# Performance work log

Hardware: AMD Instinct MI355X
Metric: run time of the kernel (lower is better)

Reference implementation:

```python
import jax, jax.numpy as jnp
import numpy as np

EMB = 256
T = 32          # block_size (hardcoded causal mask length)
HEAD = 128      # total head_size
NH = 8          # n_heads
DH = HEAD // NH # 16 per-head size
B = 4096
EPS = 1e-5


def _ln(x, g, b):
    mu = jnp.mean(x, -1, keepdims=True)
    var = jnp.var(x, -1, keepdims=True)
    return (x - mu) * jax.lax.rsqrt(var + EPS) * g + b


def setup_inputs() -> dict:
    key = jax.random.key(0)
    ks = jax.random.split(key, 12)
    s_in = 1.0 / np.sqrt(EMB)
    s_h = 1.0 / np.sqrt(HEAD)
    s_ff = 1.0 / np.sqrt(4 * EMB)
    return {
        "X": jax.random.normal(ks[0], (B, T, EMB), jnp.float32),
        "ln_g": jnp.ones((EMB,), jnp.float32),
        "ln_b": jnp.zeros((EMB,), jnp.float32),
        # per-head Q/K/V projections packed: [EMB, HEAD] == concat of NH [EMB, DH] heads
        "Wq": jax.random.uniform(ks[1], (EMB, HEAD), jnp.float32, -s_in, s_in),
        "bq": jax.random.uniform(ks[2], (HEAD,), jnp.float32, -s_in, s_in),
        "Wk": jax.random.uniform(ks[3], (EMB, HEAD), jnp.float32, -s_in, s_in),
        "bk": jax.random.uniform(ks[4], (HEAD,), jnp.float32, -s_in, s_in),
        "Wv": jax.random.uniform(ks[5], (EMB, HEAD), jnp.float32, -s_in, s_in),
        "bv": jax.random.uniform(ks[6], (HEAD,), jnp.float32, -s_in, s_in),
        "Wo": jax.random.uniform(ks[7], (HEAD, EMB), jnp.float32, -s_h, s_h),
        "bo": jax.random.uniform(ks[8], (EMB,), jnp.float32, -s_h, s_h),
        "W1": jax.random.uniform(ks[9], (EMB, 4 * EMB), jnp.float32, -s_in, s_in),
        "b1": jax.random.uniform(ks[10], (4 * EMB,), jnp.float32, -s_in, s_in),
        "W2": jax.random.uniform(ks[11], (4 * EMB, EMB), jnp.float32, -s_ff, s_ff),
        "b2": jax.random.uniform(jax.random.fold_in(key, 99), (EMB,), jnp.float32, -s_ff, s_ff),
    }


def reference(X, ln_g, ln_b, Wq, bq, Wk, bk, Wv, bv, Wo, bo, W1, b1, W2, b2):
    h = _ln(X, ln_g, ln_b)                              # [B,T,E]
    # packed QKV, split into heads: [B,T,NH,DH]
    Q = (h @ Wq + bq).reshape(B, T, NH, DH)
    K = (h @ Wk + bk).reshape(B, T, NH, DH)
    V = (h @ Wv + bv).reshape(B, T, NH, DH)
    scores = jnp.einsum("bqhd,bkhd->bhqk", Q, K)        # [B,NH,T,T]
    mask = jnp.tril(jnp.ones((T, T), bool))
    # original: masked_fill(-inf) then divide by sqrt(dh); -inf unchanged
    scores = jnp.where(mask, scores / np.sqrt(DH), -jnp.inf)
    attn = jax.nn.softmax(scores, -1)
    ctx = jnp.einsum("bhqk,bkhd->bqhd", attn, V).reshape(B, T, HEAD)
    X = ctx @ Wo + bo + X                               # residual 1
    h2 = _ln(X, ln_g, ln_b)                             # shared LN params
    out = jax.nn.relu(h2 @ W1 + b1) @ W2 + b2 + X       # residual 2
    return out
```

## Files before the change

kernel.cpp:

```cpp
#include <hip/hip_runtime.h>
#include <math.h>

typedef __attribute__((ext_vector_type(8))) __bf16 bf16x8;
typedef __attribute__((ext_vector_type(8))) unsigned short u16x8;
typedef __attribute__((ext_vector_type(4))) unsigned short u16x4;
typedef __attribute__((ext_vector_type(4))) float f32x4;

namespace {
constexpr int EMB = 256;
constexpr int HD  = 128;
constexpr int FF  = 1024;
constexpr float EPSV = 1e-5f;
constexpr int M   = 64;

constexpr int WS_QKV = 0;
constexpr int WS_O   = 98304;
constexpr int WS_1   = 131072;
constexpr int WS_2   = 393216;

__device__ __forceinline__ unsigned short f32_to_bf16(float f) {
    unsigned int u = __builtin_bit_cast(unsigned int, f);
    u += 0x7FFFu + ((u >> 16) & 1u);
    return (unsigned short)(u >> 16);
}
__device__ __forceinline__ float bf16_to_f32(unsigned short h) {
    return __builtin_bit_cast(float, ((unsigned int)h) << 16);
}
__device__ __forceinline__ f32x4 mfma16(u16x8 a, u16x8 b, f32x4 c) {
    return __builtin_amdgcn_mfma_f32_16x16x32_bf16(
        __builtin_bit_cast(bf16x8, a), __builtin_bit_cast(bf16x8, b), c, 0, 0, 0);
}
__device__ __forceinline__ int swzB(int row) { return (row & 7) << 4; }

__device__ __forceinline__ u16x8 ldsA256(const unsigned short* base, int row, int k0) {
    int byte = (row * 256 + k0 * 2) ^ swzB(row);
    return *(const u16x8*)((const char*)base + byte);
}
__device__ __forceinline__ u16x8 ldsA512(const unsigned short* base, int row, int k0) {
    int byte = (row * 512 + k0 * 2) ^ swzB(row);
    return *(const u16x8*)((const char*)base + byte);
}
__device__ __forceinline__ u16x8 ldgF(const unsigned short* base, int frag, int lane) {
    return *(const u16x8*)(base + ((size_t)frag * 64 + lane) * 8);
}
}

__global__ __launch_bounds__(256) void wconv(
    const float* __restrict__ Wq, const float* __restrict__ Wk, const float* __restrict__ Wv,
    const float* __restrict__ Wo, const float* __restrict__ W1, const float* __restrict__ W2,
    unsigned short* __restrict__ ws) {
    int e = blockIdx.x * 256 + threadIdx.x;
    int j, lane, kk, nt, n, k;
    float v;
    if (e < WS_O) {
        int t = e; j = t & 7; lane = (t >> 3) & 63; int r2 = t >> 9;
        kk = r2 & 7; nt = r2 >> 3;
        n = nt * 16 + (lane & 15); k = kk * 32 + (lane >> 4) * 8 + j;
        const float* W = (n < 128) ? Wq : ((n < 256) ? Wk : Wv);
        v = W[k * HD + (n & 127)];
    } else if (e < WS_1) {
        int t = e - WS_O; j = t & 7; lane = (t >> 3) & 63; int r2 = t >> 9;
        kk = r2 & 3; nt = r2 >> 2;
        n = nt * 16 + (lane & 15); k = kk * 32 + (lane >> 4) * 8 + j;
        v = Wo[k * EMB + n];
    } else if (e < WS_2) {
        int t = e - WS_1; j = t & 7; lane = (t >> 3) & 63; int r2 = t >> 9;
        kk = r2 & 7; nt = r2 >> 3;
        n = nt * 16 + (lane & 15); k = kk * 32 + (lane >> 4) * 8 + j;
        v = W1[k * FF + n];
    } else {
        int t = e - WS_2; j = t & 7; lane = (t >> 3) & 63; int r2 = t >> 9;
        kk = r2 & 31; nt = r2 >> 5;
        n = nt * 16 + (lane & 15); k = kk * 32 + (lane >> 4) * 8 + j;
        v = W2[k * EMB + n];
    }
    ws[e] = f32_to_bf16(v);
}

__global__ __launch_bounds__(256, 1) void attn_block_mfma(
    const float* __restrict__ X, const float* __restrict__ ln_g, const float* __restrict__ ln_b,
    const float* __restrict__ bq, const float* __restrict__ bk, const float* __restrict__ bv,
    const float* __restrict__ bo, const float* __restrict__ b1, const float* __restrict__ b2,
    const unsigned short* __restrict__ ws, float* __restrict__ out) {
    __shared__ __attribute__((aligned(16))) char smem[81920];
    unsigned short* hbuf = (unsigned short*)smem;
    unsigned short* Qb   = (unsigned short*)(smem + 32768);
    char* Kc             = smem + 49152;
    char* Vc             = smem + 65536;
    unsigned short* X1b  = (unsigned short*)(smem + 49152);
    unsigned short* fch  = Qb;

    const unsigned short* WTqkv = ws + WS_QKV;
    const unsigned short* WTo   = ws + WS_O;
    const unsigned short* WT1   = ws + WS_1;
    const unsigned short* WT2   = ws + WS_2;

    const int tid  = threadIdx.x;
    const int wv   = tid >> 6;
    const int lane = tid & 63;
    const int lr   = lane & 15;
    const int lh   = lane >> 4;
    const int row0 = blockIdx.x * M;
    const f32x4 Z  = {0.f, 0.f, 0.f, 0.f};

    {
        const int r = tid >> 3, sub = tid & 7;
        #pragma unroll 1
        for (int pass = 0; pass < 2; ++pass) {
            int rr = pass * 32 + r;
            const float* xr = X + (size_t)(row0 + rr) * EMB;
            float4 vv[8];
            float s = 0.f, ss = 0.f;
            #pragma unroll
            for (int j = 0; j < 8; ++j) {
                float4 v = *(const float4*)&xr[sub * 4 + j * 32];
                vv[j] = v;
                s  += (v.x + v.y) + (v.z + v.w);
                ss += (v.x * v.x + v.y * v.y) + (v.z * v.z + v.w * v.w);
            }
            #pragma unroll
            for (int w = 1; w < 8; w <<= 1) { s += __shfl_xor(s, w, 64); ss += __shfl_xor(ss, w, 64); }
            float mu  = s * (1.f / EMB);
            float inv = rsqrtf(fmaxf(ss * (1.f / EMB) - mu * mu, 0.f) + EPSV);
            #pragma unroll
            for (int j = 0; j < 8; ++j) {
                int c = sub * 4 + j * 32;
                float4 v = vv[j];
                float4 g4 = *(const float4*)&ln_g[c];
                float4 b4 = *(const float4*)&ln_b[c];
                u16x4 pk;
                pk[0] = f32_to_bf16((v.x - mu) * inv * g4.x + b4.x);
                pk[1] = f32_to_bf16((v.y - mu) * inv * g4.y + b4.y);
                pk[2] = f32_to_bf16((v.z - mu) * inv * g4.z + b4.z);
                pk[3] = f32_to_bf16((v.w - mu) * inv * g4.w + b4.w);
                *(u16x4*)((char*)hbuf + ((rr * 512 + c * 2) ^ swzB(rr))) = pk;
            }
        }
    }
    __syncthreads();

    {
        #pragma unroll 1
        for (int mtp = 0; mtp < 4; mtp += 2) {
            u16x8 afr[2][8];
            #pragma unroll
            for (int m = 0; m < 2; ++m)
                #pragma unroll
                for (int kk = 0; kk < 8; ++kk)
                    afr[m][kk] = ldsA512(hbuf, (mtp + m) * 16 + lr, kk * 32 + lh * 8);
            #pragma unroll 1
            for (int i = 0; i < 6; ++i) {
                int nt = wv * 6 + i;
                u16x8 bfr[8];
                #pragma unroll
                for (int kk = 0; kk < 8; ++kk) bfr[kk] = ldgF(WTqkv, nt * 8 + kk, lane);
                int gcol = nt * 16 + lr;
                int mat = gcol >> 7, c = gcol & 127;
                const float* bias = (mat == 0) ? bq : ((mat == 1) ? bk : bv);
                float bc = bias[c];
                char* regbase = smem + 32768 + mat * 16384;
                #pragma unroll
                for (int m = 0; m < 2; ++m) {
                    f32x4 e = Z, o = Z;
                    #pragma unroll
                    for (int kk = 0; kk < 8; kk += 2) {
                        e = mfma16(afr[m][kk], bfr[kk], e);
                        o = mfma16(afr[m][kk + 1], bfr[kk + 1], o);
                    }
                    f32x4 a = e + o;
                    #pragma unroll
                    for (int reg = 0; reg < 4; ++reg) {
                        int r0 = (mtp + m) * 16 + lh * 4 + reg;
                        *(unsigned short*)(regbase + ((r0 * 256 + c * 2) ^ swzB(r0))) =
                            f32_to_bf16(a[reg] + bc);
                    }
                }
            }
        }
    }
    __syncthreads();

    {
        const int hd = (tid >> 5) & 7, q = tid & 31;
        #pragma unroll 1
        for (int s = 0; s < 2; ++s) {
            int row = s * 32 + q;
            int by0 = (row * 256 + hd * 32) ^ swzB(row);
            int by1 = (row * 256 + hd * 32 + 16) ^ swzB(row);
            float qreg[16];
            {
                u16x8 a = *(const u16x8*)((const char*)Qb + by0);
                u16x8 b_ = *(const u16x8*)((const char*)Qb + by1);
                #pragma unroll
                for (int j = 0; j < 8; ++j) { qreg[j] = bf16_to_f32(a[j]); qreg[8 + j] = bf16_to_f32(b_[j]); }
            }
            float p[32]; float mmax = -1e30f;
            #pragma unroll
            for (int k = 0; k < 32; ++k) {
                int rk = s * 32 + k;
                int kb0 = (rk * 256 + hd * 32) ^ swzB(rk);
                int kb1 = (rk * 256 + hd * 32 + 16) ^ swzB(rk);
                u16x8 a = *(const u16x8*)(Kc + kb0);
                u16x8 b_ = *(const u16x8*)(Kc + kb1);
                float s_ = 0.f;
                #pragma unroll
                for (int j = 0; j < 8; ++j)
                    s_ += qreg[j] * bf16_to_f32(a[j]) + qreg[8 + j] * bf16_to_f32(b_[j]);
                s_ *= 0.25f;
                p[k] = s_;
                if (k <= q) mmax = fmaxf(mmax, s_);
            }
            float den = 0.f;
            #pragma unroll
            for (int k = 0; k < 32; ++k) {
                float e = (k <= q) ? __expf(p[k] - mmax) : 0.f;
                p[k] = e; den += e;
            }
            float rd = 1.f / den;
            float ctx[16];
            #pragma unroll
            for (int j = 0; j < 16; ++j) ctx[j] = 0.f;
            #pragma unroll
            for (int k = 0; k < 32; ++k) {
                int rk = s * 32 + k;
                int vb0 = (rk * 256 + hd * 32) ^ swzB(rk);
                int vb1 = (rk * 256 + hd * 32 + 16) ^ swzB(rk);
                u16x8 a = *(const u16x8*)(Vc + vb0);
                u16x8 b_ = *(const u16x8*)(Vc + vb1);
                float pk_ = p[k];
                #pragma unroll
                for (int j = 0; j < 8; ++j) { ctx[j] += pk_ * bf16_to_f32(a[j]); ctx[8 + j] += pk_ * bf16_to_f32(b_[j]); }
            }
            u16x8 o0, o1;
            #pragma unroll
            for (int j = 0; j < 8; ++j) { o0[j] = f32_to_bf16(ctx[j] * rd); o1[j] = f32_to_bf16(ctx[8 + j] * rd); }
            *(u16x8*)((char*)Qb + by0) = o0;
            *(u16x8*)((char*)Qb + by1) = o1;
        }
    }
    __syncthreads();

    {
        u16x8 afr[4][4];
        #pragma unroll
        for (int mt = 0; mt < 4; ++mt)
            #pragma unroll
            for (int kk = 0; kk < 4; ++kk)
                afr[mt][kk] = ldsA256(Qb, mt * 16 + lr, kk * 32 + lh * 8);
        #pragma unroll 1
        for (int i = 0; i < 4; ++i) {
            int nt = wv * 4 + i;
            u16x8 bfr[4];
            #pragma unroll
            for (int kk = 0; kk < 4; ++kk) bfr[kk] = ldgF(WTo, nt * 4 + kk, lane);
            int col = nt * 16 + lr;
            float bc = bo[col];
            #pragma unroll
            for (int mt = 0; mt < 4; ++mt) {
                f32x4 e = Z, o = Z;
                e = mfma16(afr[mt][0], bfr[0], e);
                o = mfma16(afr[mt][1], bfr[1], o);
                e = mfma16(afr[mt][2], bfr[2], e);
                o = mfma16(afr[mt][3], bfr[3], o);
                f32x4 a = e + o;
                #pragma unroll
                for (int reg = 0; reg < 4; ++reg) {
                    int r0 = mt * 16 + lh * 4 + reg;
                    float xv = X[(size_t)(row0 + r0) * EMB + col];
                    *(unsigned short*)((char*)X1b + ((r0 * 512 + col * 2) ^ swzB(r0))) =
                        f32_to_bf16(a[reg] + bc + xv);
                }
            }
        }
    }
    __syncthreads();

    {
        const int r = tid >> 3, sub = tid & 7;
        #pragma unroll 1
        for (int pass = 0; pass < 2; ++pass) {
            int rr = pass * 32 + r;
            float vals[32];
            float s = 0.f, ss = 0.f;
            #pragma unroll
            for (int j = 0; j < 8; ++j) {
                int c = sub * 4 + j * 32;
                u16x4 hv = *(const u16x4*)((const char*)X1b + ((rr * 512 + c * 2) ^ swzB(rr)));
                #pragma unroll
                for (int t = 0; t < 4; ++t) {
                    float f = bf16_to_f32(hv[t]);
                    vals[j * 4 + t] = f;
                    s += f; ss += f * f;
                }
            }
            #pragma unroll
            for (int w = 1; w < 8; w <<= 1) { s += __shfl_xor(s, w, 64); ss += __shfl_xor(ss, w, 64); }
            float mu  = s * (1.f / EMB);
            float inv = rsqrtf(fmaxf(ss * (1.f / EMB) - mu * mu, 0.f) + EPSV);
            #pragma unroll
            for (int j = 0; j < 8; ++j) {
                int c = sub * 4 + j * 32;
                float4 g4 = *(const float4*)&ln_g[c];
                float4 b4 = *(const float4*)&ln_b[c];
                u16x4 pk;
                pk[0] = f32_to_bf16((vals[j * 4 + 0] - mu) * inv * g4.x + b4.x);
                pk[1] = f32_to_bf16((vals[j * 4 + 1] - mu) * inv * g4.y + b4.y);
                pk[2] = f32_to_bf16((vals[j * 4 + 2] - mu) * inv * g4.z + b4.z);
                pk[3] = f32_to_bf16((vals[j * 4 + 3] - mu) * inv * g4.w + b4.w);
                *(u16x4*)((char*)hbuf + ((rr * 512 + c * 2) ^ swzB(rr))) = pk;
            }
        }
    }
    __syncthreads();

    {
        f32x4 acc2[4][4];
        #pragma unroll
        for (int mt = 0; mt < 4; ++mt)
            #pragma unroll
            for (int i = 0; i < 4; ++i) acc2[mt][i] = Z;

        #pragma unroll 1
        for (int ch = 0; ch < 8; ++ch) {
            #pragma unroll 1
            for (int mtp = 0; mtp < 4; mtp += 2) {
                u16x8 afr[2][8];
                #pragma unroll
                for (int m = 0; m < 2; ++m)
                    #pragma unroll
                    for (int kk = 0; kk < 8; ++kk)
                        afr[m][kk] = ldsA512(hbuf, (mtp + m) * 16 + lr, kk * 32 + lh * 8);
                #pragma unroll
                for (int f = 0; f < 2; ++f) {
                    int fn = ch * 8 + wv * 2 + f;
                    u16x8 bAll[8];
                    #pragma unroll
                    for (int kk = 0; kk < 8; ++kk) bAll[kk] = ldgF(WT1, fn * 8 + kk, lane);
                    float bc = b1[fn * 16 + lr];
                    int cc = (wv * 2 + f) * 16 + lr;
                    #pragma unroll
                    for (int m = 0; m < 2; ++m) {
                        f32x4 e = Z, o = Z;
                        #pragma unroll
                        for (int kk = 0; kk < 8; kk += 2) {
                            e = mfma16(afr[m][kk], bAll[kk], e);
                            o = mfma16(afr[m][kk + 1], bAll[kk + 1], o);
                        }
                        f32x4 a = e + o;
                        #pragma unroll
                        for (int reg = 0; reg < 4; ++reg) {
                            int r0 = (mtp + m) * 16 + lh * 4 + reg;
                            *(unsigned short*)((char*)fch + ((r0 * 256 + cc * 2) ^ swzB(r0))) =
                                f32_to_bf16(fmaxf(a[reg] + bc, 0.f));
                        }
                    }
                }
            }
            __syncthreads();
            u16x8 b2f[4][4];
            #pragma unroll
            for (int i = 0; i < 4; ++i)
                #pragma unroll
                for (int kk = 0; kk < 4; ++kk)
                    b2f[i][kk] = ldgF(WT2, (wv * 4 + i) * 32 + ch * 4 + kk, lane);
            #pragma unroll
            for (int mt = 0; mt < 4; ++mt) {
                u16x8 afr[4];
                #pragma unroll
                for (int kk = 0; kk < 4; ++kk)
                    afr[kk] = ldsA256(fch, mt * 16 + lr, kk * 32 + lh * 8);
                #pragma unroll
                for (int i = 0; i < 4; ++i) {
                    f32x4 t = acc2[mt][i];
                    t = mfma16(afr[0], b2f[i][0], t);
                    t = mfma16(afr[1], b2f[i][1], t);
                    t = mfma16(afr[2], b2f[i][2], t);
                    t = mfma16(afr[3], b2f[i][3], t);
                    acc2[mt][i] = t;
                }
            }
            __syncthreads();
        }
        float* outp = out + (size_t)row0 * EMB;
        #pragma unroll
        for (int i = 0; i < 4; ++i) {
            int col = (wv * 4 + i) * 16 + lr;
            float bc = b2[col];
            #pragma unroll
            for (int mt = 0; mt < 4; ++mt) {
                #pragma unroll
                for (int reg = 0; reg < 4; ++reg) {
                    int r0 = mt * 16 + lh * 4 + reg;
                    float x1 = bf16_to_f32(*(const unsigned short*)((const char*)X1b +
                                          ((r0 * 512 + col * 2) ^ swzB(r0))));
                    outp[(size_t)r0 * EMB + col] = acc2[mt][i][reg] + bc + x1;
                }
            }
        }
    }
}

extern "C" void kernel_launch(void* const* d_in, const int* in_sizes, int n_in,
                              void* d_out, int out_size, void* d_ws, size_t ws_size,
                              hipStream_t stream) {
    const float* X    = (const float*)d_in[0];
    const float* ln_g = (const float*)d_in[1];
    const float* ln_b = (const float*)d_in[2];
    const float* Wq   = (const float*)d_in[3];
    const float* bq   = (const float*)d_in[4];
    const float* Wk   = (const float*)d_in[5];
    const float* bk   = (const float*)d_in[6];
    const float* Wv   = (const float*)d_in[7];
    const float* bv   = (const float*)d_in[8];
    const float* Wo   = (const float*)d_in[9];
    const float* bo   = (const float*)d_in[10];
    const float* W1   = (const float*)d_in[11];
    const float* b1   = (const float*)d_in[12];
    const float* W2   = (const float*)d_in[13];
    const float* b2   = (const float*)d_in[14];
    unsigned short* ws = (unsigned short*)d_ws;
    float* O = (float*)d_out;

    wconv<<<2560, 256, 0, stream>>>(Wq, Wk, Wv, Wo, W1, W2, ws);
    attn_block_mfma<<<2048, 256, 0, stream>>>(X, ln_g, ln_b, bq, bk, bv, bo, b1, b2, ws, O);
}
```

Before: 431.6 us.

## Split fused block into attention and FFN kernels with smaller per-kernel LDS

Splits the single fused kernel into two: an attention kernel that handles one 32-row sequence per block and writes the fp32 residual X1 to the output buffer, and an FFN kernel that reads X1 back from global memory, applies LayerNorm and the MLP, and adds the residual in place. Each kernel uses much less LDS (40KB and 48KB instead of 80KB), so more workgroups can be resident per CU. This costs an extra global round-trip of the B*T*EMB fp32 intermediate and one more launch. It also replaces the manual bf16 rounding with a native __bf16 conversion and keeps X1 in fp32 rather than bf16, which slightly changes numerics.

Measured after the change: 500.2 us. +15.9%, slower.

```diff
diff --git a/kernel.cpp b/kernel.cpp
--- a/kernel.cpp
+++ b/kernel.cpp
@@ -11,7 +11,6 @@
 constexpr int HD  = 128;
 constexpr int FF  = 1024;
 constexpr float EPSV = 1e-5f;
-constexpr int M   = 64;
 
 constexpr int WS_QKV = 0;
 constexpr int WS_O   = 98304;
@@ -19,9 +18,7 @@
 constexpr int WS_2   = 393216;
 
 __device__ __forceinline__ unsigned short f32_to_bf16(float f) {
-    unsigned int u = __builtin_bit_cast(unsigned int, f);
-    u += 0x7FFFu + ((u >> 16) & 1u);
-    return (unsigned short)(u >> 16);
+    return __builtin_bit_cast(unsigned short, (__bf16)f);
 }
 __device__ __forceinline__ float bf16_to_f32(unsigned short h) {
     return __builtin_bit_cast(float, ((unsigned int)h) << 16);
@@ -77,30 +74,203 @@
     ws[e] = f32_to_bf16(v);
 }
 
-__global__ __launch_bounds__(256, 1) void attn_block_mfma(
+__global__ __launch_bounds__(256, 1) void attn_part(
     const float* __restrict__ X, const float* __restrict__ ln_g, const float* __restrict__ ln_b,
     const float* __restrict__ bq, const float* __restrict__ bk, const float* __restrict__ bv,
-    const float* __restrict__ bo, const float* __restrict__ b1, const float* __restrict__ b2,
-    const unsigned short* __restrict__ ws, float* __restrict__ out) {
-    __shared__ __attribute__((aligned(16))) char smem[81920];
-    unsigned short* hbuf = (unsigned short*)smem;
-    unsigned short* Qb   = (unsigned short*)(smem + 32768);
-    char* Kc             = smem + 49152;
-    char* Vc             = smem + 65536;
-    unsigned short* X1b  = (unsigned short*)(smem + 49152);
-    unsigned short* fch  = Qb;
+    const float* __restrict__ bo, const unsigned short* __restrict__ ws,
+    float* __restrict__ x1out) {
+    __shared__ __attribute__((aligned(16))) char smem[40960];
+    unsigned short* hb = (unsigned short*)smem;
+    unsigned short* Qb = (unsigned short*)(smem + 16384);
+    char* Kc           = smem + 24576;
+    char* Vc           = smem + 32768;
 
     const unsigned short* WTqkv = ws + WS_QKV;
     const unsigned short* WTo   = ws + WS_O;
-    const unsigned short* WT1   = ws + WS_1;
-    const unsigned short* WT2   = ws + WS_2;
 
     const int tid  = threadIdx.x;
     const int wv   = tid >> 6;
     const int lane = tid & 63;
     const int lr   = lane & 15;
     const int lh   = lane >> 4;
-    const int row0 = blockIdx.x * M;
+    const int row0 = blockIdx.x * 32;
+    const f32x4 Z  = {0.f, 0.f, 0.f, 0.f};
+
+    {
+        const int r = tid >> 3, sub = tid & 7;
+        const float* xr = X + (size_t)(row0 + r) * EMB;
+        float4 vv[8];
+        float s = 0.f, ss = 0.f;
+        #pragma unroll
+        for (int j = 0; j < 8; ++j) {
+            float4 v = *(const float4*)&xr[sub * 4 + j * 32];
+            vv[j] = v;
+            s  += (v.x + v.y) + (v.z + v.w);
+            ss += (v.x * v.x + v.y * v.y) + (v.z * v.z + v.w * v.w);
+        }
+        #pragma unroll
+        for (int w = 1; w < 8; w <<= 1) { s += __shfl_xor(s, w, 64); ss += __shfl_xor(ss, w, 64); }
+        float mu  = s * (1.f / EMB);
+        float inv = rsqrtf(fmaxf(ss * (1.f / EMB) - mu * mu, 0.f) + EPSV);
+        #pragma unroll
+        for (int j = 0; j < 8; ++j) {
+            int c = sub * 4 + j * 32;
+            float4 v = vv[j];
+            float4 g4 = *(const float4*)&ln_g[c];
+            float4 b4 = *(const float4*)&ln_b[c];
+            u16x4 pk;
+            pk[0] = f32_to_bf16((v.x - mu) * inv * g4.x + b4.x);
+            pk[1] = f32_to_bf16((v.y - mu) * inv * g4.y + b4.y);
+            pk[2] = f32_to_bf16((v.z - mu) * inv * g4.z + b4.z);
+            pk[3] = f32_to_bf16((v.w - mu) * inv * g4.w + b4.w);
+            *(u16x4*)((char*)hb + ((r * 512 + c * 2) ^ swzB(r))) = pk;
+        }
+    }
+    __syncthreads();
+
+    {
+        u16x8 afr[2][8];
+        #pragma unroll
+        for (int m = 0; m < 2; ++m)
+            #pragma unroll
+            for (int kk = 0; kk < 8; ++kk)
+                afr[m][kk] = ldsA512(hb, m * 16 + lr, kk * 32 + lh * 8);
+        #pragma unroll 1
+        for (int i = 0; i < 6; ++i) {
+            int nt = wv * 6 + i;
+            u16x8 bfr[8];
+            #pragma unroll
+            for (int kk = 0; kk < 8; ++kk) bfr[kk] = ldgF(WTqkv, nt * 8 + kk, lane);
+            int gcol = nt * 16 + lr;
+            int mat = gcol >> 7, c = gcol & 127;
+            const float* bias = (mat == 0) ? bq : ((mat == 1) ? bk : bv);
+            float bc = bias[c];
+            char* regbase = smem + 16384 + mat * 8192;
+            #pragma unroll
+            for (int m = 0; m < 2; ++m) {
+                f32x4 e = Z, o = Z;
+                #pragma unroll
+                for (int kk = 0; kk < 8; kk += 2) {
+                    e = mfma16(afr[m][kk], bfr[kk], e);
+                    o = mfma16(afr[m][kk + 1], bfr[kk + 1], o);
+                }
+                f32x4 a = e + o;
+                #pragma unroll
+                for (int reg = 0; reg < 4; ++reg) {
+                    int r0 = m * 16 + lh * 4 + reg;
+                    *(unsigned short*)(regbase + ((r0 * 256 + c * 2) ^ swzB(r0))) =
+                        f32_to_bf16(a[reg] + bc);
+                }
+            }
+        }
+    }
+    __syncthreads();
+
+    {
+        const int hd = tid >> 5, q = tid & 31;
+        int by0 = (q * 256 + hd * 32) ^ swzB(q);
+        int by1 = (q * 256 + hd * 32 + 16) ^ swzB(q);
+        float qreg[16];
+        {
+            u16x8 a = *(const u16x8*)((const char*)Qb + by0);
+            u16x8 b_ = *(const u16x8*)((const char*)Qb + by1);
+            #pragma unroll
+            for (int j = 0; j < 8; ++j) { qreg[j] = bf16_to_f32(a[j]); qreg[8 + j] = bf16_to_f32(b_[j]); }
+        }
+        float p[32]; float mmax = -1e30f;
+        #pragma unroll
+        for (int k = 0; k < 32; ++k) {
+            int kb0 = (k * 256 + hd * 32) ^ swzB(k);
+            int kb1 = (k * 256 + hd * 32 + 16) ^ swzB(k);
+            u16x8 a = *(const u16x8*)(Kc + kb0);
+            u16x8 b_ = *(const u16x8*)(Kc + kb1);
+            float s_ = 0.f;
+            #pragma unroll
+            for (int j = 0; j < 8; ++j)
+                s_ += qreg[j] * bf16_to_f32(a[j]) + qreg[8 + j] * bf16_to_f32(b_[j]);
+            s_ *= 0.25f;
+            p[k] = s_;
+            if (k <= q) mmax = fmaxf(mmax, s_);
+        }
+        float den = 0.f;
+        #pragma unroll
+        for (int k = 0; k < 32; ++k) {
+            float e = (k <= q) ? __expf(p[k] - mmax) : 0.f;
+            p[k] = e; den += e;
+        }
+        float rd = 1.f / den;
+        float ctx[16];
+        #pragma unroll
+        for (int j = 0; j < 16; ++j) ctx[j] = 0.f;
+        #pragma unroll
+        for (int k = 0; k < 32; ++k) {
+            int vb0 = (k * 256 + hd * 32) ^ swzB(k);
+            int vb1 = (k * 256 + hd * 32 + 16) ^ swzB(k);
+            u16x8 a = *(const u16x8*)(Vc + vb0);
+            u16x8 b_ = *(const u16x8*)(Vc + vb1);
+            float pk_ = p[k];
+            #pragma unroll
+            for (int j = 0; j < 8; ++j) { ctx[j] += pk_ * bf16_to_f32(a[j]); ctx[8 + j] += pk_ * bf16_to_f32(b_[j]); }
+        }
+        u16x8 o0, o1;
+        #pragma unroll
+        for (int j = 0; j < 8; ++j) { o0[j] = f32_to_bf16(ctx[j] * rd); o1[j] = f32_to_bf16(ctx[8 + j] * rd); }
+        *(u16x8*)((char*)Qb + by0) = o0;
+        *(u16x8*)((char*)Qb + by1) = o1;
+    }
+    __syncthreads();
+
+    {
+        u16x8 afr[2][4];
+        #pragma unroll
+        for (int m = 0; m < 2; ++m)
+            #pragma unroll
+            for (int kk = 0; kk < 4; ++kk)
+                afr[m][kk] = ldsA256(Qb, m * 16 + lr, kk * 32 + lh * 8);
+        #pragma unroll 1
+        for (int i = 0; i < 4; ++i) {
+            int nt = wv * 4 + i;
+            u16x8 bfr[4];
+            #pragma unroll
+            for (int kk = 0; kk < 4; ++kk) bfr[kk] = ldgF(WTo, nt * 4 + kk, lane);
+            int col = nt * 16 + lr;
+            float bc = bo[col];
+            #pragma unroll
+            for (int m = 0; m < 2; ++m) {
+                f32x4 e = Z, o = Z;
+                e = mfma16(afr[m][0], bfr[0], e);
+                o = mfma16(afr[m][1], bfr[1], o);
+                e = mfma16(afr[m][2], bfr[2], e);
+                o = mfma16(afr[m][3], bfr[3], o);
+                f32x4 a = e + o;
+                #pragma unroll
+                for (int reg = 0; reg < 4; ++reg) {
+                    int r0 = m * 16 + lh * 4 + reg;
+                    size_t gi = (size_t)(row0 + r0) * EMB + col;
+                    x1out[gi] = a[reg] + bc + X[gi];
+                }
+            }
+        }
+    }
+}
+
+__global__ __launch_bounds__(256, 1) void ffn_part(
+    const float* __restrict__ ln_g, const float* __restrict__ ln_b,
+    const float* __restrict__ b1, const float* __restrict__ b2,
+    const unsigned short* __restrict__ ws, float* __restrict__ io) {
+    __shared__ __attribute__((aligned(16))) char smem[49152];
+    unsigned short* h2  = (unsigned short*)smem;
+    unsigned short* fch = (unsigned short*)(smem + 32768);
+
+    const unsigned short* WT1 = ws + WS_1;
+    const unsigned short* WT2 = ws + WS_2;
+
+    const int tid  = threadIdx.x;
+    const int wv   = tid >> 6;
+    const int lane = tid & 63;
+    const int lr   = lane & 15;
+    const int lh   = lane >> 4;
+    const int row0 = blockIdx.x * 64;
     const f32x4 Z  = {0.f, 0.f, 0.f, 0.f};
 
     {
@@ -108,7 +278,7 @@
         #pragma unroll 1
         for (int pass = 0; pass < 2; ++pass) {
             int rr = pass * 32 + r;
-            const float* xr = X + (size_t)(row0 + rr) * EMB;
+            const float* xr = io + (size_t)(row0 + rr) * EMB;
             float4 vv[8];
             float s = 0.f, ss = 0.f;
             #pragma unroll
@@ -133,255 +303,78 @@
                 pk[1] = f32_to_bf16((v.y - mu) * inv * g4.y + b4.y);
                 pk[2] = f32_to_bf16((v.z - mu) * inv * g4.z + b4.z);
                 pk[3] = f32_to_bf16((v.w - mu) * inv * g4.w + b4.w);
-                *(u16x4*)((char*)hbuf + ((rr * 512 + c * 2) ^ swzB(rr))) = pk;
+                *(u16x4*)((char*)h2 + ((rr * 512 + c * 2) ^ swzB(rr))) = pk;
             }
         }
     }
     __syncthreads();
 
     {
+        f32x4 acc2[4][4];
+        #pragma unroll
+        for (int mt = 0; mt < 4; ++mt)
+            #pragma unroll
+            for (int i = 0; i < 4; ++i) acc2[mt][i] = Z;
+
         #pragma unroll 1
-        for (int mtp = 0; mtp < 4; mtp += 2) {
-            u16x8 afr[2][8];
-            #pragma unroll
-            for (int m = 0; m < 2; ++m)
-                #pragma unroll
-                for (int kk = 0; kk < 8; ++kk)
-                    afr[m][kk] = ldsA512(hbuf, (mtp + m) * 16 + lr, kk * 32 + lh * 8);
-            #pragma unroll 1
-            for (int i = 0; i < 6; ++i) {
-                int nt = wv * 6 + i;
-                u16x8 bfr[8];
-                #pragma unroll
-                for (int kk = 0; kk < 8; ++kk) bfr[kk] = ldgF(WTqkv, nt * 8 + kk, lane);
-                int gcol = nt * 16 + lr;
-                int mat = gcol >> 7, c = gcol & 127;
-                const float* bias = (mat == 0) ? bq : ((mat == 1) ? bk : bv);
-                float bc = bias[c];
-                char* regbase = smem + 32768 + mat * 16384;
-                #pragma unroll
-                for (int m = 0; m < 2; ++m) {
+        for (int ch = 0; ch < 8; ++ch) {
+            #pragma unroll
+            for (int f = 0; f < 2; ++f) {
+                int fn = ch * 8 + wv * 2 + f;
+                u16x8 bAll[8];
+                #pragma unroll
+                for (int kk = 0; kk < 8; ++kk) bAll[kk] = ldgF(WT1, fn * 8 + kk, lane);
+                float bc = b1[fn * 16 + lr];
+                int cc = (wv * 2 + f) * 16 + lr;
+                #pragma unroll 1
+                for (int mt = 0; mt < 4; ++mt) {
+                    u16x8 afr[8];
+                    #pragma unroll
+                    for (int kk = 0; kk < 8; ++kk)
+                        afr[kk] = ldsA512(h2, mt * 16 + lr, kk * 32 + lh * 8);
                     f32x4 e = Z, o = Z;
                     #pragma unroll
                     for (int kk = 0; kk < 8; kk += 2) {
-                        e = mfma16(afr[m][kk], bfr[kk], e);
-                        o = mfma16(afr[m][kk + 1], bfr[kk + 1], o);
+                        e = mfma16(afr[kk], bAll[kk], e);
+                        o = mfma16(afr[kk + 1], bAll[kk + 1], o);
                     }
                     f32x4 a = e + o;
                     #pragma unroll
                     for (int reg = 0; reg < 4; ++reg) {
-                        int r0 = (mtp + m) * 16 + lh * 4 + reg;
-                        *(unsigned short*)(regbase + ((r0 * 256 + c * 2) ^ swzB(r0))) =
-                            f32_to_bf16(a[reg] + bc);
+                        int r0 = mt * 16 + lh * 4 + reg;
+                        *(unsigned short*)((char*)fch + ((r0 * 256 + cc * 2) ^ swzB(r0))) =
+                            f32_to_bf16(fmaxf(a[reg] + bc, 0.f));
                     }
                 }
             }
-        }
-    }
-    __syncthreads();
-
-    {
-        const int hd = (tid >> 5) & 7, q = tid & 31;
-        #pragma unroll 1
-        for (int s = 0; s < 2; ++s) {
-            int row = s * 32 + q;
-            int by0 = (row * 256 + hd * 32) ^ swzB(row);
-            int by1 = (row * 256 + hd * 32 + 16) ^ swzB(row);
-            float qreg[16];
-            {
-                u16x8 a = *(const u16x8*)((const char*)Qb + by0);
-                u16x8 b_ = *(const u16x8*)((const char*)Qb + by1);
-                #pragma unroll
-                for (int j = 0; j < 8; ++j) { qreg[j] = bf16_to_f32(a[j]); qreg[8 + j] = bf16_to_f32(b_[j]); }
-            }
-            float p[32]; float mmax = -1e30f;
-            #pragma unroll
-            for (int k = 0; k < 32; ++k) {
-                int rk = s * 32 + k;
-                int kb0 = (rk * 256 + hd * 32) ^ swzB(rk);
-                int kb1 = (rk * 256 + hd * 32 + 16) ^ swzB(rk);
-                u16x8 a = *(const u16x8*)(Kc + kb0);
-                u16x8 b_ = *(const u16x8*)(Kc + kb1);
-                float s_ = 0.f;
-                #pragma unroll
-                for (int j = 0; j < 8; ++j)
-                    s_ += qreg[j] * bf16_to_f32(a[j]) + qreg[8 + j] * bf16_to_f32(b_[j]);
-                s_ *= 0.25f;
-                p[k] = s_;
-                if (k <= q) mmax = fmaxf(mmax, s_);
-            }
-            float den = 0.f;
-            #pragma unroll
-            for (int k = 0; k < 32; ++k) {
-                float e = (k <= q) ? __expf(p[k] - mmax) : 0.f;
-                p[k] = e; den += e;
-            }
-            float rd = 1.f / den;
-            float ctx[16];
-            #pragma unroll
-            for (int j = 0; j < 16; ++j) ctx[j] = 0.f;
-            #pragma unroll
-            for (int k = 0; k < 32; ++k) {
-                int rk = s * 32 + k;
-                int vb0 = (rk * 256 + hd * 32) ^ swzB(rk);
-                int vb1 = (rk * 256 + hd * 32 + 16) ^ swzB(rk);
-                u16x8 a = *(const u16x8*)(Vc + vb0);
-                u16x8 b_ = *(const u16x8*)(Vc + vb1);
-                float pk_ = p[k];
-                #pragma unroll
-                for (int j = 0; j < 8; ++j) { ctx[j] += pk_ * bf16_to_f32(a[j]); ctx[8 + j] += pk_ * bf16_to_f32(b_[j]); }
-            }
-            u16x8 o0, o1;
-            #pragma unroll
-            for (int j = 0; j < 8; ++j) { o0[j] = f32_to_bf16(ctx[j] * rd); o1[j] = f32_to_bf16(ctx[8 + j] * rd); }
-            *(u16x8*)((char*)Qb + by0) = o0;
-            *(u16x8*)((char*)Qb + by1) = o1;
-        }
-    }
-    __syncthreads();
-
-    {
-        u16x8 afr[4][4];
-        #pragma unroll
-        for (int mt = 0; mt < 4; ++mt)
-            #pragma unroll
-            for (int kk = 0; kk < 4; ++kk)
-                afr[mt][kk] = ldsA256(Qb, mt * 16 + lr, kk * 32 + lh * 8);
-        #pragma unroll 1
-        for (int i = 0; i < 4; ++i) {
-            int nt = wv * 4 + i;
-            u16x8 bfr[4];
-            #pragma unroll
-            for (int kk = 0; kk < 4; ++kk) bfr[kk] = ldgF(WTo, nt * 4 + kk, lane);
-            int col = nt * 16 + lr;
-            float bc = bo[col];
-            #pragma unroll
-            for (int mt = 0; mt < 4; ++mt) {
-                f32x4 e = Z, o = Z;
-                e = mfma16(afr[mt][0], bfr[0], e);
-                o = mfma16(afr[mt][1], bfr[1], o);
-                e = mfma16(afr[mt][2], bfr[2], e);
-                o = mfma16(afr[mt][3], bfr[3], o);
-                f32x4 a = e + o;
-                #pragma unroll
-                for (int reg = 0; reg < 4; ++reg) {
-                    int r0 = mt * 16 + lh * 4 + reg;
-                    float xv = X[(size_t)(row0 + r0) * EMB + col];
-                    *(unsigned short*)((char*)X1b + ((r0 * 512 + col * 2) ^ swzB(r0))) =
-                        f32_to_bf16(a[reg] + bc + xv);
-                }
-            }
-        }
-    }
-    __syncthreads();
-
-    {
-        const int r = tid >> 3, sub = tid & 7;
-        #pragma unroll 1
-        for (int pass = 0; pass < 2; ++pass) {
-            int rr = pass * 32 + r;
-            float vals[32];
-            float s = 0.f, ss = 0.f;
-            #pragma unroll
-            for (int j = 0; j < 8; ++j) {
-                int c = sub * 4 + j * 32;
-                u16x4 hv = *(const u16x4*)((const char*)X1b + ((rr * 512 + c * 2) ^ swzB(rr)));
-                #pragma unroll
-                for (int t = 0; t < 4; ++t) {
-                    float f = bf16_to_f32(hv[t]);
-                    vals[j * 4 + t] = f;
-                    s += f; ss += f * f;
-                }
-            }
-            #pragma unroll
-            for (int w = 1; w < 8; w <<= 1) { s += __shfl_xor(s, w, 64); ss += __shfl_xor(ss, w, 64); }
-            float mu  = s * (1.f / EMB);
-            float inv = rsqrtf(fmaxf(ss * (1.f / EMB) - mu * mu, 0.f) + EPSV);
-            #pragma unroll
-            for (int j = 0; j < 8; ++j) {
-                int c = sub * 4 + j * 32;
-                float4 g4 = *(const float4*)&ln_g[c];
-                float4 b4 = *(const float4*)&ln_b[c];
-                u16x4 pk;
-                pk[0] = f32_to_bf16((vals[j * 4 + 0] - mu) * inv * g4.x + b4.x);
-                pk[1] = f32_to_bf16((vals[j * 4 + 1] - mu) * inv * g4.y + b4.y);
-                pk[2] = f32_to_bf16((vals[j * 4 + 2] - mu) * inv * g4.z + b4.z);
-                pk[3] = f32_to_bf16((vals[j * 4 + 3] - mu) * inv * g4.w + b4.w);
-                *(u16x4*)((char*)hbuf + ((rr * 512 + c * 2) ^ swzB(rr))) = pk;
-            }
-        }
-    }
-    __syncthreads();
-
-    {
-        f32x4 acc2[4][4];
-        #pragma unroll
-        for (int mt = 0; mt < 4; ++mt)
-            #pragma unroll
-            for (int i = 0; i < 4; ++i) acc2[mt][i] = Z;
-
-        #pragma unroll 1
-        for (int ch = 0; ch < 8; ++ch) {
-            #pragma unroll 1
-            for (int mtp = 0; mtp < 4; mtp += 2) {
-                u16x8 afr[2][8];
-                #pragma unroll
-                for (int m = 0; m < 2; ++m)
-                    #pragma unroll
-                    for (int kk = 0; kk < 8; ++kk)
-                        afr[m][kk] = ldsA512(hbuf, (mtp + m) * 16 + lr, kk * 32 + lh * 8);
-                #pragma unroll
-                for (int f = 0; f < 2; ++f) {
-                    int fn = ch * 8 + wv * 2 + f;
-                    u16x8 bAll[8];
-                    #pragma unroll
-                    for (int kk = 0; kk < 8; ++kk) bAll[kk] = ldgF(WT1, fn * 8 + kk, lane);
-                    float bc = b1[fn * 16 + lr];
-                    int cc = (wv * 2 + f) * 16 + lr;
-                    #pragma unroll
-                    for (int m = 0; m < 2; ++m) {
-                        f32x4 e = Z, o = Z;
-                        #pragma unroll
-                        for (int kk = 0; kk < 8; kk += 2) {
-                            e = mfma16(afr[m][kk], bAll[kk], e);
-                            o = mfma16(afr[m][kk + 1], bAll[kk + 1], o);
-                        }
-                        f32x4 a = e + o;
-                        #pragma unroll
-                        for (int reg = 0; reg < 4; ++reg) {
-                            int r0 = (mtp + m) * 16 + lh * 4 + reg;
-                            *(unsigned short*)((char*)fch + ((r0 * 256 + cc * 2) ^ swzB(r0))) =
-                                f32_to_bf16(fmaxf(a[reg] + bc, 0.f));
-                        }
+            __syncthreads();
+            #pragma unroll
+            for (int half = 0; half < 2; ++half) {
+                u16x8 b2f[2][4];
+                #pragma unroll
+                for (int i = 0; i < 2; ++i)
+                    #pragma unroll
+                    for (int kk = 0; kk < 4; ++kk)
+                        b2f[i][kk] = ldgF(WT2, (wv * 4 + half * 2 + i) * 32 + ch * 4 + kk, lane);
+                #pragma unroll
+                for (int mt = 0; mt < 4; ++mt) {
+                    u16x8 afr[4];
+                    #pragma unroll
+                    for (int kk = 0; kk < 4; ++kk)
+                        afr[kk] = ldsA256(fch, mt * 16 + lr, kk * 32 + lh * 8);
+                    #pragma unroll
+                    for (int i = 0; i < 2; ++i) {
+                        f32x4 t = acc2[mt][half * 2 + i];
+                        t = mfma16(afr[0], b2f[i][0], t);
+                        t = mfma16(afr[1], b2f[i][1], t);
+                        t = mfma16(afr[2], b2f[i][2], t);
+                        t = mfma16(afr[3], b2f[i][3], t);
+                        acc2[mt][half * 2 + i] = t;
                     }
                 }
             }
             __syncthreads();
-            u16x8 b2f[4][4];
-            #pragma unroll
-            for (int i = 0; i < 4; ++i)
-                #pragma unroll
-                for (int kk = 0; kk < 4; ++kk)
-                    b2f[i][kk] = ldgF(WT2, (wv * 4 + i) * 32 + ch * 4 + kk, lane);
-            #pragma unroll
-            for (int mt = 0; mt < 4; ++mt) {
-                u16x8 afr[4];
-                #pragma unroll
-                for (int kk = 0; kk < 4; ++kk)
-                    afr[kk] = ldsA256(fch, mt * 16 + lr, kk * 32 + lh * 8);
-                #pragma unroll
-                for (int i = 0; i < 4; ++i) {
-                    f32x4 t = acc2[mt][i];
-                    t = mfma16(afr[0], b2f[i][0], t);
-                    t = mfma16(afr[1], b2f[i][1], t);
-                    t = mfma16(afr[2], b2f[i][2], t);
-                    t = mfma16(afr[3], b2f[i][3], t);
-                    acc2[mt][i] = t;
-                }
-            }
-            __syncthreads();
-        }
-        float* outp = out + (size_t)row0 * EMB;
+        }
         #pragma unroll
         for (int i = 0; i < 4; ++i) {
             int col = (wv * 4 + i) * 16 + lr;
@@ -391,9 +384,8 @@
                 #pragma unroll
                 for (int reg = 0; reg < 4; ++reg) {
                     int r0 = mt * 16 + lh * 4 + reg;
-                    float x1 = bf16_to_f32(*(const unsigned short*)((const char*)X1b +
-                                          ((r0 * 512 + col * 2) ^ swzB(r0))));
-                    outp[(size_t)r0 * EMB + col] = acc2[mt][i][reg] + bc + x1;
+                    size_t gi = (size_t)(row0 + r0) * EMB + col;
+                    io[gi] = acc2[mt][i][reg] + bc + io[gi];
                 }
             }
         }
@@ -422,5 +414,6 @@
     float* O = (float*)d_out;
 
     wconv<<<2560, 256, 0, stream>>>(Wq, Wk, Wv, Wo, W1, W2, ws);
-    attn_block_mfma<<<2048, 256, 0, stream>>>(X, ln_g, ln_b, bq, bk, bv, bo, b1, b2, ws, O);
-}
+    attn_part<<<4096, 256, 0, stream>>>(X, ln_g, ln_b, bq, bk, bv, bo, ws, O);
+    ffn_part<<<2048, 256, 0, stream>>>(ln_g, ln_b, b1, b2, ws, O);
+}
```
